# Optimization experiments

Hardware: AMD Instinct MI355X
Metric: run time of the kernel (lower is better)

Reference implementation:

```python
import jax, jax.numpy as jnp
import numpy as np


def setup_inputs() -> dict:
    key = jax.random.key(0)
    k1, k2, k3 = jax.random.split(key, 3)
    B, N, D = 4, 4096, 256
    val = jax.random.normal(k1, (B, N, D), dtype=jnp.float32)
    state = jax.random.normal(k2, (B, N), dtype=jnp.float32)
    # val projection weight, scaled for unit-variance outputs
    Wv = jax.random.normal(k3, (D, D), dtype=jnp.float32) / np.sqrt(D)
    return {"val": val, "state": state, "Wv": Wv}


def reference(val, state, Wv):
    # pairwise_fn: dot-product scores over all node pairs -> [B, N, N]
    scores = jnp.einsum("bnd,bmd->bnm", val, val)
    # edge_compress_fn: softsign (non-softmax elementwise nonlinearity)
    edges = scores / (1.0 + jnp.abs(scores))
    # state_proj_fn = identity, val_proj_fn = linear
    projected_state = state                                  # [B, N]
    projected_val = jnp.einsum("bmd,de->bme", val, Wv)       # [B, N, D]
    # dual aggregation reusing the same edge matrix
    delta_state = jnp.einsum("bnm,bm->bn", edges, projected_state)
    delta_val = jnp.einsum("bnm,bmd->bnd", edges, projected_val)
    return (delta_state, delta_val)
```

## Files before the change

kernel.cpp:

```cpp
#include <hip/hip_runtime.h>

typedef unsigned short u16;
typedef unsigned char u8;
typedef unsigned int u32;
typedef __bf16 bf16x8 __attribute__((ext_vector_type(8)));
typedef float  f32x16 __attribute__((ext_vector_type(16)));
typedef int    i32x4  __attribute__((ext_vector_type(4)));
typedef int    i32x16 __attribute__((ext_vector_type(16)));

#define NB 4
#define NN 4096
#define ND 256

#define QPV (127.0f / 4.5f)
#define DPV (4.5f / 16129.0f)
#define QST (127.0f / 4.6f)
#define DST (4.6f / 16129.0f)
#define MAGIC 12582912.0f

__device__ __forceinline__ u16 f2bf(float x) { return __builtin_bit_cast(u16, (__bf16)x); }
__device__ __forceinline__ u32 fbits(float x) { return __builtin_bit_cast(u32, x); }

__device__ __forceinline__ u32 packlow4(float a, float b, float c, float d) {
    u32 p = __builtin_amdgcn_perm(fbits(b), fbits(a), 0x00000400u);
    u32 q = __builtin_amdgcn_perm(fbits(d), fbits(c), 0x00000400u);
    return __builtin_amdgcn_perm(q, p, 0x05040100u);
}


__global__ __launch_bounds__(256) void k_wv(const float* __restrict__ Wv, u16* __restrict__ wv) {
    __shared__ u16 t2[256 * 33];
    int tid = threadIdx.x;
    int es = blockIdx.x, e0 = es * 32;
    #pragma unroll
    for (int k = 0; k < 8; k++) {
        int idx = tid + k * 256;
        int row = idx >> 3, c4 = idx & 7;
        float4 v = *(const float4*)(Wv + row * 256 + e0 + c4 * 4);
        u16* p = t2 + row * 33 + c4 * 4;
        p[0] = f2bf(v.x); p[1] = f2bf(v.y); p[2] = f2bf(v.z); p[3] = f2bf(v.w);
    }
    __syncthreads();
    u16* dst = wv + (size_t)es * 16 * 512;
    #pragma unroll
    for (int k = 0; k < 4; k++) {
        int flat = tid + k * 256;
        int s = flat >> 6, l = flat & 63;
        int l31 = l & 31, h = l >> 5;
        union { u16 o[8]; uint4 q; } u;
        #pragma unroll
        for (int j = 0; j < 8; j++) u.o[j] = t2[(s * 16 + h * 8 + j) * 33 + l31];
        *(uint4*)(dst + (size_t)flat * 8) = u.q;
    }
}

__global__ __launch_bounds__(256) void k_prep(const float* __restrict__ val,
                                              const float* __restrict__ state,
                                              const u16* __restrict__ wvf,
                                              u8* __restrict__ kq8,
                                              float* __restrict__ srow,
                                              u8* __restrict__ vp8) {
    int tid = threadIdx.x;
    int bid = blockIdx.x;
    if (bid < 512) {
        __shared__ float t[32 * 257];
        __shared__ float rmax[32];
        __shared__ u8 tp[4][32 * 48];
        const float* src = val + (size_t)bid * 32 * 256;
        #pragma unroll
        for (int k = 0; k < 8; k++) {
            int idx = tid + k * 256;
            int row = idx >> 6, c4 = idx & 63;
            float4 v = *(const float4*)(src + row * 256 + c4 * 4);
            float* p = t + row * 257 + c4 * 4;
            p[0] = v.x; p[1] = v.y; p[2] = v.z; p[3] = v.w;
        }
        __syncthreads();
        {
            int row = tid >> 3, seg = tid & 7;
            float m = 0.0f;
            #pragma unroll
            for (int i = 0; i < 32; i++) m = fmaxf(m, fabsf(t[row * 257 + seg + i * 8]));
            m = fmaxf(m, __shfl_down(m, 4));
            m = fmaxf(m, __shfl_down(m, 2));
            m = fmaxf(m, __shfl_down(m, 1));
            if (seg == 0) {
                m = fmaxf(m, 1e-20f);
                rmax[row] = m;
                srow[bid * 32 + row] = m * (1.0f / 127.0f);
            }
        }
        __syncthreads();
        u8* dst8 = kq8 + (size_t)bid * 8192;
        #pragma unroll
        for (int k = 0; k < 2; k++) {
            int flat = tid + k * 256;
            int s = flat >> 6, l = flat & 63;
            int l31 = l & 31, h = l >> 5;
            float r127 = 127.0f / rmax[l31];
            const float* p = t + l31 * 257 + s * 32 + h * 16;
            u32 d[4];
            #pragma unroll
            for (int g = 0; g < 4; g++)
                d[g] = packlow4(fmaf(p[4 * g + 0], r127, MAGIC), fmaf(p[4 * g + 1], r127, MAGIC),
                                fmaf(p[4 * g + 2], r127, MAGIC), fmaf(p[4 * g + 3], r127, MAGIC));
            *(uint4*)(dst8 + (size_t)flat * 16) = make_uint4(d[0], d[1], d[2], d[3]);
        }
        {
            int w = tid >> 6, lane = tid & 63;
            int l31 = lane & 31, h = lane >> 5;
            const u16* wv0 = wvf + ((size_t)((w * 2 + 0) * 16)) * 512 + lane * 8;
            const u16* wv1 = wvf + ((size_t)((w * 2 + 1) * 16)) * 512 + lane * 8;
            f32x16 acc0 = {}, acc1 = {};
            for (int s = 0; s < 16; s++) {
                union { u16 o[8]; bf16x8 v; } ua;
                const float* p = t + l31 * 257 + s * 16 + h * 8;
                #pragma unroll
                for (int j = 0; j < 8; j++) ua.o[j] = f2bf(p[j]);
                bf16x8 b0 = *(const bf16x8*)(wv0 + (size_t)s * 512);
                bf16x8 b1 = *(const bf16x8*)(wv1 + (size_t)s * 512);
                acc0 = __builtin_amdgcn_mfma_f32_32x32x16_bf16(ua.v, b0, acc0, 0, 0, 0);
                acc1 = __builtin_amdgcn_mfma_f32_32x32x16_bf16(ua.v, b1, acc1, 0, 0, 0);
            }
            u8* myp = tp[w];
            #pragma unroll
            for (int r = 0; r < 16; r++) {
                int nrow = (r & 3) + 8 * (r >> 2) + 4 * h;
                float x = fminf(fmaxf(acc0[r] * QPV, -127.0f), 127.0f);
                myp[l31 * 48 + nrow] = (u8)(fbits(x + MAGIC) & 255);
            }
            i32x4 v0 = *(const i32x4*)(myp + l31 * 48 + h * 16);
            *(i32x4*)(vp8 + ((size_t)(bid * 9 + w * 2 + 0)) * 1024 + lane * 16) = v0;
            #pragma unroll
            for (int r = 0; r < 16; r++) {
                int nrow = (r & 3) + 8 * (r >> 2) + 4 * h;
                float x = fminf(fmaxf(acc1[r] * QPV, -127.0f), 127.0f);
                myp[l31 * 48 + nrow] = (u8)(fbits(x + MAGIC) & 255);
            }
            i32x4 v1 = *(const i32x4*)(myp + l31 * 48 + h * 16);
            *(i32x4*)(vp8 + ((size_t)(bid * 9 + w * 2 + 1)) * 1024 + lane * 16) = v1;
        }
    } else {
        int b = bid - 512;
        __shared__ u8 qs[4096];
        #pragma unroll
        for (int k = 0; k < 16; k++) {
            int i = tid + k * 256;
            float x = fminf(fmaxf(state[b * 4096 + i] * QST, -127.0f), 127.0f);
            qs[i] = (u8)(fbits(x + MAGIC) & 255);
        }
        __syncthreads();
        #pragma unroll
        for (int k = 0; k < 32; k++) {
            int chunk = tid + k * 256;
            int strip = chunk >> 6, lane = chunk & 63, h = (lane >> 5) & 1;
            i32x4 v = *(const i32x4*)(qs + strip * 32 + h * 16);
            *(i32x4*)(vp8 + ((size_t)((b * 128 + strip) * 9 + 8)) * 1024 + (chunk & 63) * 16) = v;
        }
    }
}

__global__ __launch_bounds__(256, 2) void k_main(const u8* __restrict__ kq8,
                                                 const u8* __restrict__ vp8,
                                                 const float* __restrict__ srow,
                                                 float* __restrict__ ds_out,
                                                 float* __restrict__ dval_out) {
    __shared__ i32x4 pbuf[2][4][64];
    __shared__ int dsqi[4][32];

    int tid = threadIdx.x;
    int w = tid >> 6, lane = tid & 63;
    int l31 = lane & 31, h = lane >> 5;

    int id = blockIdx.x;
    int xcd = id & 7;
    int bb = xcd >> 1;
    int t7 = ((xcd & 1) << 6) | (id >> 3);
    int q0 = t7 * 32;
    size_t bbase = (size_t)bb * 128;

    i32x4 qf[8];
    {
        const u8* qsrc = kq8 + (bbase + t7) * 8192 + lane * 16;
        #pragma unroll
        for (int s = 0; s < 8; s++) qf[s] = *(const i32x4*)(qsrc + (size_t)s * 1024);
    }
    float srq = srow[bb * 4096 + q0 + l31];

    i32x16 oacc[2] = {};
    i32x16 dsa = {};

    i32x4 kf[8], vf[4][2], sf;
    float4 sg[4];
    {
        const u8* kb = kq8 + (bbase + w) * 8192 + lane * 16;
        #pragma unroll
        for (int s = 0; s < 8; s++) kf[s] = *(const i32x4*)(kb + (size_t)s * 1024);
        #pragma unroll
        for (int st = 0; st < 4; st++)
            #pragma unroll
            for (int e = 0; e < 2; e++)
                vf[st][e] = *(const i32x4*)(vp8 + ((size_t)((bbase + st) * 9 + 2 * w + e)) * 1024 + lane * 16);
        sf = *(const i32x4*)(vp8 + ((size_t)((bbase + w) * 9 + 8)) * 1024 + lane * 16);
        const float* srm = srow + bb * 4096 + w * 32;
        #pragma unroll
        for (int g = 0; g < 4; g++) sg[g] = *(const float4*)(srm + g * 8 + h * 4);
    }

    for (int mt = 0; mt < 32; mt++) {
        i32x16 s0 = {}, s1 = {};
        #pragma unroll
        for (int s = 0; s < 8; s += 2) {
            s0 = __builtin_amdgcn_mfma_i32_32x32x32_i8(kf[s], qf[s], s0, 0, 0, 0);
            s1 = __builtin_amdgcn_mfma_i32_32x32x32_i8(kf[s + 1], qf[s + 1], s1, 0, 0, 0);
        }
        if (mt + 1 < 32) {
            const u8* kb = kq8 + (bbase + (mt + 1) * 4 + w) * 8192 + lane * 16;
            #pragma unroll
            for (int s = 0; s < 8; s++) kf[s] = *(const i32x4*)(kb + (size_t)s * 1024);
        }

        float cf[16];
        #pragma unroll
        for (int r = 0; r < 16; r++) {
            float sm = ((const float*)&sg[r >> 2])[r & 3] * srq;
            float xs = (float)(s0[r] + s1[r]) * sm;
            float p = xs * __builtin_amdgcn_rcpf(1.0f + fabsf(xs));
            cf[r] = fmaf(p, 127.0f, MAGIC);
        }
        if (mt + 1 < 32) {
            const float* srm = srow + bb * 4096 + (mt + 1) * 128 + w * 32;
            #pragma unroll
            for (int g = 0; g < 4; g++) sg[g] = *(const float4*)(srm + g * 8 + h * 4);
        }
        u32 w0 = packlow4(cf[0], cf[1], cf[2], cf[3]);
        u32 w1 = packlow4(cf[4], cf[5], cf[6], cf[7]);
        u32 w2 = packlow4(cf[8], cf[9], cf[10], cf[11]);
        u32 w3 = packlow4(cf[12], cf[13], cf[14], cf[15]);
        u32 x0 = (u32)__shfl_xor((int)w0, 32);
        u32 x1 = (u32)__shfl_xor((int)w1, 32);
        u32 x2 = (u32)__shfl_xor((int)w2, 32);
        u32 x3 = (u32)__shfl_xor((int)w3, 32);
        union { u32 wd[4]; i32x4 v; } pu;
        if (h == 0) { pu.wd[0] = w0; pu.wd[1] = x0; pu.wd[2] = w1; pu.wd[3] = x1; }
        else        { pu.wd[0] = x2; pu.wd[1] = w2; pu.wd[2] = x3; pu.wd[3] = w3; }
        i32x4 pf = pu.v;

        dsa = __builtin_amdgcn_mfma_i32_32x32x32_i8(pf, sf, dsa, 0, 0, 0);
        if (mt + 1 < 32)
            sf = *(const i32x4*)(vp8 + ((size_t)((bbase + (mt + 1) * 4 + w) * 9 + 8)) * 1024 + lane * 16);

        pbuf[mt & 1][w][lane] = pf;
        __syncthreads();
        i32x4 pl[4];
        #pragma unroll
        for (int st = 0; st < 4; st++) pl[st] = pbuf[mt & 1][st][lane];

        #pragma unroll
        for (int st = 0; st < 4; st++) {
            oacc[0] = __builtin_amdgcn_mfma_i32_32x32x32_i8(pl[st], vf[st][0], oacc[0], 0, 0, 0);
            oacc[1] = __builtin_amdgcn_mfma_i32_32x32x32_i8(pl[st], vf[st][1], oacc[1], 0, 0, 0);
        }
        if (mt + 1 < 32) {
            #pragma unroll
            for (int st = 0; st < 4; st++)
                #pragma unroll
                for (int e = 0; e < 2; e++)
                    vf[st][e] = *(const i32x4*)(vp8 + ((size_t)((bbase + (mt + 1) * 4 + st) * 9 + 2 * w + e)) * 1024 + lane * 16);
        }
    }

    if (l31 == 0) {
        #pragma unroll
        for (int r = 0; r < 16; r++) dsqi[w][(r & 3) + 8 * (r >> 2) + 4 * h] = dsa[r];
    }
    #pragma unroll
    for (int e = 0; e < 2; e++) {
        #pragma unroll
        for (int r = 0; r < 16; r++) {
            int row = (r & 3) + 8 * (r >> 2) + 4 * h;
            dval_out[((size_t)(bb * 4096 + q0 + row)) * 256 + (2 * w + e) * 32 + l31] =
                (float)oacc[e][r] * DPV;
        }
    }
    __syncthreads();
    if (w == 0 && lane < 32) {
        int d = dsqi[0][lane] + dsqi[1][lane] + dsqi[2][lane] + dsqi[3][lane];
        ds_out[bb * 4096 + q0 + lane] = (float)d * DST;
    }
}

extern "C" void kernel_launch(void* const* d_in, const int* in_sizes, int n_in,
                              void* d_out, int out_size, void* d_ws, size_t ws_size,
                              hipStream_t stream) {
    const float* val   = (const float*)d_in[0];
    const float* state = (const float*)d_in[1];
    const float* Wv    = (const float*)d_in[2];

    float* ds_out   = (float*)d_out;
    float* dval_out = ds_out + NB * NN;

    u8*  kq8 = (u8*)d_ws;
    u8*  vp8 = kq8 + (size_t)NB * NN * ND;
    u16* wv  = (u16*)(vp8 + (size_t)NB * 128 * 9216);
    float* srow = (float*)(wv + 8 * 16 * 512);

    k_wv<<<8, 256, 0, stream>>>(Wv, wv);
    k_prep<<<516, 256, 0, stream>>>(val, state, wv, kq8, srow, vp8);
    k_main<<<512, 256, 0, stream>>>(kq8, vp8, srow, ds_out, dval_out);
}
```

Before: 136.9 us.

## Use 8 waves per block, each owning one 32-column output slice

The main kernel goes from 4 to 8 waves per block. Each wave now handles one 32-wide slice of the value output instead of two, and the loop covers 8 key strips per iteration over 16 iterations instead of 4 strips over 32. This halves the trips through the loop and the block barriers, and gives more waves to hide latency. In exchange each wave holds 8 value fragments plus two accumulators, and launch bounds of 512 threads with 4 blocks per CU may force register spills or limit residency.

After: 440.6 us. +221.8%, slower.

```diff
diff --git a/kernel.cpp b/kernel.cpp
--- a/kernel.cpp
+++ b/kernel.cpp
@@ -160,13 +160,13 @@
     }
 }
 
-__global__ __launch_bounds__(256, 2) void k_main(const u8* __restrict__ kq8,
+__global__ __launch_bounds__(512, 4) void k_main(const u8* __restrict__ kq8,
                                                  const u8* __restrict__ vp8,
                                                  const float* __restrict__ srow,
                                                  float* __restrict__ ds_out,
                                                  float* __restrict__ dval_out) {
-    __shared__ i32x4 pbuf[2][4][64];
-    __shared__ int dsqi[4][32];
+    __shared__ i32x4 pbuf[2][8][64];
+    __shared__ int dsqi[8][32];
 
     int tid = threadIdx.x;
     int w = tid >> 6, lane = tid & 63;
@@ -187,35 +187,33 @@
     }
     float srq = srow[bb * 4096 + q0 + l31];
 
-    i32x16 oacc[2] = {};
+    i32x16 oa = {}, ob = {};
     i32x16 dsa = {};
 
-    i32x4 kf[8], vf[4][2], sf;
+    i32x4 kf[8], vf[8], sf;
     float4 sg[4];
     {
         const u8* kb = kq8 + (bbase + w) * 8192 + lane * 16;
         #pragma unroll
         for (int s = 0; s < 8; s++) kf[s] = *(const i32x4*)(kb + (size_t)s * 1024);
         #pragma unroll
-        for (int st = 0; st < 4; st++)
-            #pragma unroll
-            for (int e = 0; e < 2; e++)
-                vf[st][e] = *(const i32x4*)(vp8 + ((size_t)((bbase + st) * 9 + 2 * w + e)) * 1024 + lane * 16);
+        for (int st = 0; st < 8; st++)
+            vf[st] = *(const i32x4*)(vp8 + ((size_t)((bbase + st) * 9 + w)) * 1024 + lane * 16);
         sf = *(const i32x4*)(vp8 + ((size_t)((bbase + w) * 9 + 8)) * 1024 + lane * 16);
         const float* srm = srow + bb * 4096 + w * 32;
         #pragma unroll
         for (int g = 0; g < 4; g++) sg[g] = *(const float4*)(srm + g * 8 + h * 4);
     }
 
-    for (int mt = 0; mt < 32; mt++) {
+    for (int t = 0; t < 16; t++) {
         i32x16 s0 = {}, s1 = {};
         #pragma unroll
         for (int s = 0; s < 8; s += 2) {
             s0 = __builtin_amdgcn_mfma_i32_32x32x32_i8(kf[s], qf[s], s0, 0, 0, 0);
             s1 = __builtin_amdgcn_mfma_i32_32x32x32_i8(kf[s + 1], qf[s + 1], s1, 0, 0, 0);
         }
-        if (mt + 1 < 32) {
-            const u8* kb = kq8 + (bbase + (mt + 1) * 4 + w) * 8192 + lane * 16;
+        if (t + 1 < 16) {
+            const u8* kb = kq8 + (bbase + (t + 1) * 8 + w) * 8192 + lane * 16;
             #pragma unroll
             for (int s = 0; s < 8; s++) kf[s] = *(const i32x4*)(kb + (size_t)s * 1024);
         }
@@ -228,8 +226,8 @@
             float p = xs * __builtin_amdgcn_rcpf(1.0f + fabsf(xs));
             cf[r] = fmaf(p, 127.0f, MAGIC);
         }
-        if (mt + 1 < 32) {
-            const float* srm = srow + bb * 4096 + (mt + 1) * 128 + w * 32;
+        if (t + 1 < 16) {
+            const float* srm = srow + bb * 4096 + ((t + 1) * 8 + w) * 32;
             #pragma unroll
             for (int g = 0; g < 4; g++) sg[g] = *(const float4*)(srm + g * 8 + h * 4);
         }
@@ -247,26 +245,24 @@
         i32x4 pf = pu.v;
 
         dsa = __builtin_amdgcn_mfma_i32_32x32x32_i8(pf, sf, dsa, 0, 0, 0);
-        if (mt + 1 < 32)
-            sf = *(const i32x4*)(vp8 + ((size_t)((bbase + (mt + 1) * 4 + w) * 9 + 8)) * 1024 + lane * 16);
-
-        pbuf[mt & 1][w][lane] = pf;
+        if (t + 1 < 16)
+            sf = *(const i32x4*)(vp8 + ((size_t)((bbase + (t + 1) * 8 + w) * 9 + 8)) * 1024 + lane * 16);
+
+        pbuf[t & 1][w][lane] = pf;
         __syncthreads();
-        i32x4 pl[4];
-        #pragma unroll
-        for (int st = 0; st < 4; st++) pl[st] = pbuf[mt & 1][st][lane];
+        i32x4 pl[8];
+        #pragma unroll
+        for (int st = 0; st < 8; st++) pl[st] = pbuf[t & 1][st][lane];
 
         #pragma unroll
         for (int st = 0; st < 4; st++) {
-            oacc[0] = __builtin_amdgcn_mfma_i32_32x32x32_i8(pl[st], vf[st][0], oacc[0], 0, 0, 0);
-            oacc[1] = __builtin_amdgcn_mfma_i32_32x32x32_i8(pl[st], vf[st][1], oacc[1], 0, 0, 0);
-        }
-        if (mt + 1 < 32) {
-            #pragma unroll
-            for (int st = 0; st < 4; st++)
-                #pragma unroll
-                for (int e = 0; e < 2; e++)
-                    vf[st][e] = *(const i32x4*)(vp8 + ((size_t)((bbase + (mt + 1) * 4 + st) * 9 + 2 * w + e)) * 1024 + lane * 16);
+            oa = __builtin_amdgcn_mfma_i32_32x32x32_i8(pl[st], vf[st], oa, 0, 0, 0);
+            ob = __builtin_amdgcn_mfma_i32_32x32x32_i8(pl[st + 4], vf[st + 4], ob, 0, 0, 0);
+        }
+        if (t + 1 < 16) {
+            #pragma unroll
+            for (int st = 0; st < 8; st++)
+                vf[st] = *(const i32x4*)(vp8 + ((size_t)((bbase + (t + 1) * 8 + st) * 9 + w)) * 1024 + lane * 16);
         }
     }
 
@@ -275,17 +271,15 @@
         for (int r = 0; r < 16; r++) dsqi[w][(r & 3) + 8 * (r >> 2) + 4 * h] = dsa[r];
     }
     #pragma unroll
-    for (int e = 0; e < 2; e++) {
-        #pragma unroll
-        for (int r = 0; r < 16; r++) {
-            int row = (r & 3) + 8 * (r >> 2) + 4 * h;
-            dval_out[((size_t)(bb * 4096 + q0 + row)) * 256 + (2 * w + e) * 32 + l31] =
-                (float)oacc[e][r] * DPV;
-        }
+    for (int r = 0; r < 16; r++) {
+        int row = (r & 3) + 8 * (r >> 2) + 4 * h;
+        dval_out[((size_t)(bb * 4096 + q0 + row)) * 256 + w * 32 + l31] =
+            (float)(oa[r] + ob[r]) * DPV;
     }
     __syncthreads();
     if (w == 0 && lane < 32) {
-        int d = dsqi[0][lane] + dsqi[1][lane] + dsqi[2][lane] + dsqi[3][lane];
+        int d = dsqi[0][lane] + dsqi[1][lane] + dsqi[2][lane] + dsqi[3][lane] +
+                dsqi[4][lane] + dsqi[5][lane] + dsqi[6][lane] + dsqi[7][lane];
         ds_out[bb * 4096 + q0 + lane] = (float)d * DST;
     }
 }
@@ -307,5 +301,5 @@
 
     k_wv<<<8, 256, 0, stream>>>(Wv, wv);
     k_prep<<<516, 256, 0, stream>>>(val, state, wv, kq8, srow, vp8);
-    k_main<<<512, 256, 0, stream>>>(kq8, vp8, srow, ds_out, dval_out);
-}
+    k_main<<<512, 512, 0, stream>>>(kq8, vp8, srow, ds_out, dval_out);
+}
```

## Software-pipeline score computation one tile ahead of PV accumulation

Applied to the files above, without the earlier changes.

Peels the first score tile into a prologue and restructures the main loop so the QK MFMAs and softsign packing for tile mt+1 are issued alongside the PV MFMAs for tile mt. K fragments are prefetched two tiles ahead, and the barrier moves to the end of each iteration, with the double-buffered P stored in LDS. The aim is to hide the elementwise softsign/pack latency and the barrier stall behind matrix work. The cost is higher register pressure from live score accumulators and prefetched fragments.

Result: slower. 142.4 us (+4.0%).

```diff
diff --git a/kernel.cpp b/kernel.cpp
--- a/kernel.cpp
+++ b/kernel.cpp
@@ -192,6 +192,7 @@
 
     i32x4 kf[8], vf[4][2], sf;
     float4 sg[4];
+
     {
         const u8* kb = kq8 + (bbase + w) * 8192 + lane * 16;
         #pragma unroll
@@ -205,20 +206,16 @@
         const float* srm = srow + bb * 4096 + w * 32;
         #pragma unroll
         for (int g = 0; g < 4; g++) sg[g] = *(const float4*)(srm + g * 8 + h * 4);
-    }
-
-    for (int mt = 0; mt < 32; mt++) {
+
         i32x16 s0 = {}, s1 = {};
         #pragma unroll
         for (int s = 0; s < 8; s += 2) {
             s0 = __builtin_amdgcn_mfma_i32_32x32x32_i8(kf[s], qf[s], s0, 0, 0, 0);
             s1 = __builtin_amdgcn_mfma_i32_32x32x32_i8(kf[s + 1], qf[s + 1], s1, 0, 0, 0);
         }
-        if (mt + 1 < 32) {
-            const u8* kb = kq8 + (bbase + (mt + 1) * 4 + w) * 8192 + lane * 16;
-            #pragma unroll
-            for (int s = 0; s < 8; s++) kf[s] = *(const i32x4*)(kb + (size_t)s * 1024);
-        }
+        const u8* kb1 = kq8 + (bbase + 4 + w) * 8192 + lane * 16;
+        #pragma unroll
+        for (int s = 0; s < 8; s++) kf[s] = *(const i32x4*)(kb1 + (size_t)s * 1024);
 
         float cf[16];
         #pragma unroll
@@ -227,11 +224,6 @@
             float xs = (float)(s0[r] + s1[r]) * sm;
             float p = xs * __builtin_amdgcn_rcpf(1.0f + fabsf(xs));
             cf[r] = fmaf(p, 127.0f, MAGIC);
-        }
-        if (mt + 1 < 32) {
-            const float* srm = srow + bb * 4096 + (mt + 1) * 128 + w * 32;
-            #pragma unroll
-            for (int g = 0; g < 4; g++) sg[g] = *(const float4*)(srm + g * 8 + h * 4);
         }
         u32 w0 = packlow4(cf[0], cf[1], cf[2], cf[3]);
         u32 w1 = packlow4(cf[4], cf[5], cf[6], cf[7]);
@@ -244,22 +236,38 @@
         union { u32 wd[4]; i32x4 v; } pu;
         if (h == 0) { pu.wd[0] = w0; pu.wd[1] = x0; pu.wd[2] = w1; pu.wd[3] = x1; }
         else        { pu.wd[0] = x2; pu.wd[1] = w2; pu.wd[2] = x3; pu.wd[3] = w3; }
-        i32x4 pf = pu.v;
-
-        dsa = __builtin_amdgcn_mfma_i32_32x32x32_i8(pf, sf, dsa, 0, 0, 0);
-        if (mt + 1 < 32)
-            sf = *(const i32x4*)(vp8 + ((size_t)((bbase + (mt + 1) * 4 + w) * 9 + 8)) * 1024 + lane * 16);
-
-        pbuf[mt & 1][w][lane] = pf;
-        __syncthreads();
+        dsa = __builtin_amdgcn_mfma_i32_32x32x32_i8(pu.v, sf, dsa, 0, 0, 0);
+        pbuf[0][w][lane] = pu.v;
+        sf = *(const i32x4*)(vp8 + ((size_t)((bbase + 4 + w) * 9 + 8)) * 1024 + lane * 16);
+        const float* srm1 = srow + bb * 4096 + 128 + w * 32;
+        #pragma unroll
+        for (int g = 0; g < 4; g++) sg[g] = *(const float4*)(srm1 + g * 8 + h * 4);
+    }
+    __syncthreads();
+
+    for (int mt = 0; mt < 32; mt++) {
         i32x4 pl[4];
         #pragma unroll
         for (int st = 0; st < 4; st++) pl[st] = pbuf[mt & 1][st][lane];
 
+        i32x16 s0 = {}, s1 = {};
+        if (mt + 1 < 32) {
+            #pragma unroll
+            for (int s = 0; s < 8; s += 2) {
+                s0 = __builtin_amdgcn_mfma_i32_32x32x32_i8(kf[s], qf[s], s0, 0, 0, 0);
+                s1 = __builtin_amdgcn_mfma_i32_32x32x32_i8(kf[s + 1], qf[s + 1], s1, 0, 0, 0);
+            }
+        }
         #pragma unroll
         for (int st = 0; st < 4; st++) {
             oacc[0] = __builtin_amdgcn_mfma_i32_32x32x32_i8(pl[st], vf[st][0], oacc[0], 0, 0, 0);
             oacc[1] = __builtin_amdgcn_mfma_i32_32x32x32_i8(pl[st], vf[st][1], oacc[1], 0, 0, 0);
+        }
+
+        if (mt + 2 < 32) {
+            const u8* kb = kq8 + (bbase + (mt + 2) * 4 + w) * 8192 + lane * 16;
+            #pragma unroll
+            for (int s = 0; s < 8; s++) kf[s] = *(const i32x4*)(kb + (size_t)s * 1024);
         }
         if (mt + 1 < 32) {
             #pragma unroll
@@ -268,6 +276,37 @@
                 for (int e = 0; e < 2; e++)
                     vf[st][e] = *(const i32x4*)(vp8 + ((size_t)((bbase + (mt + 1) * 4 + st) * 9 + 2 * w + e)) * 1024 + lane * 16);
         }
+
+        if (mt + 1 < 32) {
+            float cf[16];
+            #pragma unroll
+            for (int r = 0; r < 16; r++) {
+                float sm = ((const float*)&sg[r >> 2])[r & 3] * srq;
+                float xs = (float)(s0[r] + s1[r]) * sm;
+                float p = xs * __builtin_amdgcn_rcpf(1.0f + fabsf(xs));
+                cf[r] = fmaf(p, 127.0f, MAGIC);
+            }
+            u32 w0 = packlow4(cf[0], cf[1], cf[2], cf[3]);
+            u32 w1 = packlow4(cf[4], cf[5], cf[6], cf[7]);
+            u32 w2 = packlow4(cf[8], cf[9], cf[10], cf[11]);
+            u32 w3 = packlow4(cf[12], cf[13], cf[14], cf[15]);
+            u32 x0 = (u32)__shfl_xor((int)w0, 32);
+            u32 x1 = (u32)__shfl_xor((int)w1, 32);
+            u32 x2 = (u32)__shfl_xor((int)w2, 32);
+            u32 x3 = (u32)__shfl_xor((int)w3, 32);
+            union { u32 wd[4]; i32x4 v; } pu;
+            if (h == 0) { pu.wd[0] = w0; pu.wd[1] = x0; pu.wd[2] = w1; pu.wd[3] = x1; }
+            else        { pu.wd[0] = x2; pu.wd[1] = w2; pu.wd[2] = x3; pu.wd[3] = w3; }
+            dsa = __builtin_amdgcn_mfma_i32_32x32x32_i8(pu.v, sf, dsa, 0, 0, 0);
+            pbuf[(mt + 1) & 1][w][lane] = pu.v;
+            if (mt + 2 < 32) {
+                sf = *(const i32x4*)(vp8 + ((size_t)((bbase + (mt + 2) * 4 + w) * 9 + 8)) * 1024 + lane * 16);
+                const float* srm = srow + bb * 4096 + (mt + 2) * 128 + w * 32;
+                #pragma unroll
+                for (int g = 0; g < 4; g++) sg[g] = *(const float4*)(srm + g * 8 + h * 4);
+            }
+        }
+        __syncthreads();
     }
 
     if (l31 == 0) {
```

## Permute int8 K ordering so MFMA outputs pack directly into operands

Applied to the files above, without the earlier changes.

Changes the k-index ordering of the int8 operands so the accumulator layout of one MFMA can be packed straight into the A operand of the next, with no cross-half lane shuffles in the main loop. The prep kernel now writes the projected values and state in the matching permuted order, packing from registers instead of going through a shared-memory transpose. This removes four shuffles and selects per iteration in k_main and the LDS round trip in k_prep. The risk is that the new permutation must be consistent across all operands, or the results will be wrong.

New measurement: 136.6 us. About the same (-0.2%).

```diff
diff --git a/kernel.cpp b/kernel.cpp
--- a/kernel.cpp
+++ b/kernel.cpp
@@ -26,6 +26,7 @@
     u32 q = __builtin_amdgcn_perm(fbits(d), fbits(c), 0x00000400u);
     return __builtin_amdgcn_perm(q, p, 0x05040100u);
 }
+
 
 
 __global__ __launch_bounds__(256) void k_wv(const float* __restrict__ Wv, u16* __restrict__ wv) {
@@ -65,7 +66,6 @@
     if (bid < 512) {
         __shared__ float t[32 * 257];
         __shared__ float rmax[32];
-        __shared__ u8 tp[4][32 * 48];
         const float* src = val + (size_t)bid * 32 * 256;
         #pragma unroll
         for (int k = 0; k < 8; k++) {
@@ -122,23 +122,22 @@
                 acc0 = __builtin_amdgcn_mfma_f32_32x32x16_bf16(ua.v, b0, acc0, 0, 0, 0);
                 acc1 = __builtin_amdgcn_mfma_f32_32x32x16_bf16(ua.v, b1, acc1, 0, 0, 0);
             }
-            u8* myp = tp[w];
-            #pragma unroll
-            for (int r = 0; r < 16; r++) {
-                int nrow = (r & 3) + 8 * (r >> 2) + 4 * h;
-                float x = fminf(fmaxf(acc0[r] * QPV, -127.0f), 127.0f);
-                myp[l31 * 48 + nrow] = (u8)(fbits(x + MAGIC) & 255);
+            union { u32 wd[4]; i32x4 v; } o0, o1;
+            #pragma unroll
+            for (int g = 0; g < 4; g++) {
+                o0.wd[g] = packlow4(
+                    fminf(fmaxf(acc0[4 * g + 0] * QPV, -127.0f), 127.0f) + MAGIC,
+                    fminf(fmaxf(acc0[4 * g + 1] * QPV, -127.0f), 127.0f) + MAGIC,
+                    fminf(fmaxf(acc0[4 * g + 2] * QPV, -127.0f), 127.0f) + MAGIC,
+                    fminf(fmaxf(acc0[4 * g + 3] * QPV, -127.0f), 127.0f) + MAGIC);
+                o1.wd[g] = packlow4(
+                    fminf(fmaxf(acc1[4 * g + 0] * QPV, -127.0f), 127.0f) + MAGIC,
+                    fminf(fmaxf(acc1[4 * g + 1] * QPV, -127.0f), 127.0f) + MAGIC,
+                    fminf(fmaxf(acc1[4 * g + 2] * QPV, -127.0f), 127.0f) + MAGIC,
+                    fminf(fmaxf(acc1[4 * g + 3] * QPV, -127.0f), 127.0f) + MAGIC);
             }
-            i32x4 v0 = *(const i32x4*)(myp + l31 * 48 + h * 16);
-            *(i32x4*)(vp8 + ((size_t)(bid * 9 + w * 2 + 0)) * 1024 + lane * 16) = v0;
-            #pragma unroll
-            for (int r = 0; r < 16; r++) {
-                int nrow = (r & 3) + 8 * (r >> 2) + 4 * h;
-                float x = fminf(fmaxf(acc1[r] * QPV, -127.0f), 127.0f);
-                myp[l31 * 48 + nrow] = (u8)(fbits(x + MAGIC) & 255);
-            }
-            i32x4 v1 = *(const i32x4*)(myp + l31 * 48 + h * 16);
-            *(i32x4*)(vp8 + ((size_t)(bid * 9 + w * 2 + 1)) * 1024 + lane * 16) = v1;
+            *(i32x4*)(vp8 + ((size_t)(bid * 9 + w * 2 + 0)) * 1024 + lane * 16) = o0.v;
+            *(i32x4*)(vp8 + ((size_t)(bid * 9 + w * 2 + 1)) * 1024 + lane * 16) = o1.v;
         }
     } else {
         int b = bid - 512;
@@ -154,8 +153,11 @@
         for (int k = 0; k < 32; k++) {
             int chunk = tid + k * 256;
             int strip = chunk >> 6, lane = chunk & 63, h = (lane >> 5) & 1;
-            i32x4 v = *(const i32x4*)(qs + strip * 32 + h * 16);
-            *(i32x4*)(vp8 + ((size_t)((b * 128 + strip) * 9 + 8)) * 1024 + (chunk & 63) * 16) = v;
+            union { u32 wd[4]; i32x4 v; } u;
+            #pragma unroll
+            for (int g = 0; g < 4; g++)
+                u.wd[g] = *(const u32*)(qs + strip * 32 + 8 * g + 4 * h);
+            *(i32x4*)(vp8 + ((size_t)((b * 128 + strip) * 9 + 8)) * 1024 + lane * 16) = u.v;
         }
     }
 }
@@ -233,17 +235,11 @@
             #pragma unroll
             for (int g = 0; g < 4; g++) sg[g] = *(const float4*)(srm + g * 8 + h * 4);
         }
-        u32 w0 = packlow4(cf[0], cf[1], cf[2], cf[3]);
-        u32 w1 = packlow4(cf[4], cf[5], cf[6], cf[7]);
-        u32 w2 = packlow4(cf[8], cf[9], cf[10], cf[11]);
-        u32 w3 = packlow4(cf[12], cf[13], cf[14], cf[15]);
-        u32 x0 = (u32)__shfl_xor((int)w0, 32);
-        u32 x1 = (u32)__shfl_xor((int)w1, 32);
-        u32 x2 = (u32)__shfl_xor((int)w2, 32);
-        u32 x3 = (u32)__shfl_xor((int)w3, 32);
         union { u32 wd[4]; i32x4 v; } pu;
-        if (h == 0) { pu.wd[0] = w0; pu.wd[1] = x0; pu.wd[2] = w1; pu.wd[3] = x1; }
-        else        { pu.wd[0] = x2; pu.wd[1] = w2; pu.wd[2] = x3; pu.wd[3] = w3; }
+        pu.wd[0] = packlow4(cf[0], cf[1], cf[2], cf[3]);
+        pu.wd[1] = packlow4(cf[4], cf[5], cf[6], cf[7]);
+        pu.wd[2] = packlow4(cf[8], cf[9], cf[10], cf[11]);
+        pu.wd[3] = packlow4(cf[12], cf[13], cf[14], cf[15]);
         i32x4 pf = pu.v;
 
         dsa = __builtin_amdgcn_mfma_i32_32x32x32_i8(pf, sf, dsa, 0, 0, 0);
```
